# Performance work log

Measured on AMD Instinct MI355X. Metric: run time of the kernel, lower is better.

Reference implementation:

```python
import jax, jax.numpy as jnp
import numpy as np

D_MODEL = 1024
BULK_DIM = 10          # int(log2(d_model))
ADS_RADIUS = 1.0
B, N = 4, 2048


def setup_inputs() -> dict:
    key = jax.random.key(0)
    k1, k2 = jax.random.split(key, 2)
    boundary_tokens = jax.random.normal(k1, (B, N, D_MODEL), dtype=jnp.float32)
    W_b2b = jax.random.normal(k2, (D_MODEL, D_MODEL * BULK_DIM), dtype=jnp.float32) / np.sqrt(D_MODEL).astype(np.float32)
    b_b2b = jnp.zeros((D_MODEL * BULK_DIM,), dtype=jnp.float32)
    return {"boundary_tokens": boundary_tokens, "W_b2b": W_b2b, "b_b2b": b_b2b}


def _fast_marching(bulk_coords, ads_radius):
    # bulk_coords: (B, N, K, D). Sequential eikonal-style sweep through the
    # bulk depth z = 1..K; AdS warp factor L/z attenuates the front update
    # deeper into the bulk. Returns geodesics with the same shape.
    cz = jnp.moveaxis(bulk_coords, 2, 0)                 # (K, B, N, D)
    z = jnp.arange(1, bulk_coords.shape[2] + 1, dtype=bulk_coords.dtype)
    factors = ads_radius / z                             # (K,)

    def step(g, inp):
        c, f = inp
        g_new = g + f * (c - g)
        return g_new, g_new

    _, geos = jax.lax.scan(step, cz[0], (cz, factors))   # (K, B, N, D)
    return jnp.moveaxis(geos, 0, 2)                      # (B, N, K, D)


def reference(boundary_tokens, W_b2b, b_b2b):
    Bb, Nn, D = boundary_tokens.shape
    # boundary -> bulk linear projection, reshaped to (B, N, bulk_dim, D)
    bulk_coords = (boundary_tokens @ W_b2b + b_b2b).reshape(Bb, Nn, BULK_DIM, D)
    geodesics = _fast_marching(bulk_coords, ADS_RADIUS)  # (B, N, K, D)
    bulk_features = geodesics.mean(axis=2)               # (B, N, D)
    return bulk_features
```

## Files before the change

### kernel.cpp

```cpp
#include <hip/hip_runtime.h>
#include <stdint.h>


static constexpr float FW[10] = {
    0.2928968253968254f, 0.1928968253968254f, 0.1428968253968254f,
    0.1095634920634921f, 0.0845634920634921f, 0.0645634920634921f,
    0.0478968253968254f, 0.0336111111111111f, 0.0211111111111111f,
    0.0100000000000000f};

typedef __attribute__((ext_vector_type(8))) short short8;
typedef __attribute__((ext_vector_type(4))) float floatx4;

__device__ inline unsigned int bf16pack2(float hi, float lo) {
    unsigned int uh = __float_as_uint(hi) + 0x8000u;
    unsigned int ul = __float_as_uint(lo) + 0x8000u;
    return __builtin_amdgcn_perm(uh, ul, 0x07060302u);
}

#define LDS_AS(p) ((__attribute__((address_space(3))) unsigned int*)(p))
#define GLB_AS(p) ((const __attribute__((address_space(1))) unsigned int*)(p))

__global__ __launch_bounds__(256) void fold_w(const float* __restrict__ W,
                                              unsigned short* __restrict__ Wt) {
    __shared__ float T[64 * 65];
    const int t = threadIdx.x;
    const int n0 = blockIdx.x * 64;
    const int k0 = blockIdx.y * 64;

#pragma unroll
    for (int s = 0; s < 4; ++s) {
        int slot = s * 256 + t;
        int r = slot >> 4;
        int c4 = (slot & 15) * 4;
        const float4* src = (const float4*)(W + (size_t)(k0 + r) * 10240 + n0 + c4);
        float4 acc = {0.f, 0.f, 0.f, 0.f};
#pragma unroll
        for (int j = 0; j < 10; ++j) {
            float4 v = src[j * 256];
            acc.x += FW[j] * v.x; acc.y += FW[j] * v.y;
            acc.z += FW[j] * v.z; acc.w += FW[j] * v.w;
        }
        T[r * 65 + c4 + 0] = acc.x;
        T[r * 65 + c4 + 1] = acc.y;
        T[r * 65 + c4 + 2] = acc.z;
        T[r * 65 + c4 + 3] = acc.w;
    }
    __syncthreads();
#pragma unroll
    for (int s = 0; s < 4; ++s) {
        int slot = s * 256 + t;
        int nl = slot >> 4;
        int k4 = (slot & 15) * 4;
        float f0 = T[(k4 + 0) * 65 + nl];
        float f1 = T[(k4 + 1) * 65 + nl];
        float f2 = T[(k4 + 2) * 65 + nl];
        float f3 = T[(k4 + 3) * 65 + nl];
        uint2 p;
        p.x = bf16pack2(f1, f0);
        p.y = bf16pack2(f3, f2);
        *(uint2*)(Wt + (size_t)(n0 + nl) * 1024 + k0 + k4) = p;
    }
}

__global__ __launch_bounds__(256) void fold_b(const float* __restrict__ b,
                                              float* __restrict__ beff) {
    const int t = threadIdx.x;
    const float4* src = (const float4*)b + t;
    float4 acc = {0.f, 0.f, 0.f, 0.f};
#pragma unroll
    for (int j = 0; j < 10; ++j) {
        float4 v = src[j * 256];
        acc.x += FW[j] * v.x; acc.y += FW[j] * v.y;
        acc.z += FW[j] * v.z; acc.w += FW[j] * v.w;
    }
    ((float4*)beff)[t] = acc;
}

__global__ __launch_bounds__(256) void gemm_bf16(const float* __restrict__ A,
                                                 const unsigned short* __restrict__ Wt,
                                                 const float* __restrict__ beff,
                                                 float* __restrict__ C) {
    __shared__ __align__(16) unsigned short As[128 * 72];
    __shared__ __align__(16) unsigned char Bs[16384];

    const int t = threadIdx.x;
    const int lane = t & 63;
    const int w = t >> 6;
    const int quad = lane >> 4;
    const int l15 = lane & 15;
    const int wm = (w & 1) * 64;
    const int wn = (w >> 1) * 64;
    const int bm = blockIdx.y * 128;
    const int bn = blockIdx.x * 128;

    floatx4 acc[4][4];
#pragma unroll
    for (int i = 0; i < 4; ++i)
#pragma unroll
        for (int j = 0; j < 4; ++j) acc[i][j] = (floatx4){0.f, 0.f, 0.f, 0.f};

    const int ar = t >> 4;
    const int ac4 = (t & 15) * 4;
    const float* Abase = A + (size_t)(bm + ar) * 1024 + ac4;
    const char* WtB = (const char*)Wt;

    for (int k0 = 0; k0 < 1024; k0 += 64) {
#pragma unroll
        for (int i = 0; i < 4; ++i) {
            int I = w * 4 + i;
            int slot = I * 64 + lane;
            int nl = slot >> 3;
            int cs = slot & 7;
            int c = cs ^ (nl & 7);
            const char* g = WtB + (size_t)(bn + nl) * 2048 + k0 * 2 + c * 16;
            __builtin_amdgcn_global_load_lds(GLB_AS(g), LDS_AS(Bs + I * 1024), 16, 0, 0);
        }
        float4 av[8];
#pragma unroll
        for (int s = 0; s < 8; ++s)
            av[s] = *(const float4*)(Abase + (size_t)(s * 16) * 1024 + k0);
#pragma unroll
        for (int s = 0; s < 8; ++s) {
            uint2 p;
            p.x = bf16pack2(av[s].y, av[s].x);
            p.y = bf16pack2(av[s].w, av[s].z);
            *(uint2*)((char*)As + (size_t)(s * 16 + ar) * 144 + ac4 * 2) = p;
        }
        __syncthreads();

#pragma unroll
        for (int kk = 0; kk < 2; ++kk) {
            short8 af[4], bf[4];
#pragma unroll
            for (int tm = 0; tm < 4; ++tm) {
                int m = wm + tm * 16 + l15;
                af[tm] = *(const short8*)((const char*)As + (size_t)m * 144 + kk * 64 + quad * 16);
            }
#pragma unroll
            for (int tn = 0; tn < 4; ++tn) {
                int n = wn + tn * 16 + l15;
                int c = kk * 4 + quad;
                int slot = n * 8 + (c ^ (n & 7));
                bf[tn] = *(const short8*)(Bs + slot * 16);
            }
#pragma unroll
            for (int tm = 0; tm < 4; ++tm)
#pragma unroll
                for (int tn = 0; tn < 4; ++tn)
                    acc[tm][tn] = __builtin_amdgcn_mfma_f32_16x16x32_bf16(
                        af[tm], bf[tn], acc[tm][tn], 0, 0, 0);
        }
        __syncthreads();
    }

#pragma unroll
    for (int tn = 0; tn < 4; ++tn) {
        int col = bn + wn + tn * 16 + l15;
        float bias = beff[col];
#pragma unroll
        for (int tm = 0; tm < 4; ++tm) {
            int row0 = bm + wm + tm * 16 + quad * 4;
#pragma unroll
            for (int r = 0; r < 4; ++r)
                C[(size_t)(row0 + r) * 1024 + col] = acc[tm][tn][r] + bias;
        }
    }
}

extern "C" void kernel_launch(void* const* d_in, const int* in_sizes, int n_in,
                              void* d_out, int out_size, void* d_ws, size_t ws_size,
                              hipStream_t stream) {
    const float* tokens = (const float*)d_in[0];
    const float* W      = (const float*)d_in[1];
    const float* b      = (const float*)d_in[2];
    float* out = (float*)d_out;

    unsigned short* Wt = (unsigned short*)d_ws;
    float* beff = (float*)((char*)d_ws + 1024 * 1024 * 2);

    fold_w<<<dim3(16, 16), 256, 0, stream>>>(W, Wt);
    fold_b<<<1, 256, 0, stream>>>(b, beff);
    gemm_bf16<<<dim3(8, 64), 256, 0, stream>>>(tokens, Wt, beff, out);
}
```

Measured before the change: 143.3 us.

## Pre-convert activations to bf16 and load both GEMM operands via direct LDS loads

```diff
diff --git a/kernel.cpp b/kernel.cpp
--- a/kernel.cpp
+++ b/kernel.cpp
@@ -22,13 +22,13 @@
 
 __global__ __launch_bounds__(256) void fold_w(const float* __restrict__ W,
                                               unsigned short* __restrict__ Wt) {
-    __shared__ float T[64 * 65];
+    __shared__ float T[32 * 65];
     const int t = threadIdx.x;
     const int n0 = blockIdx.x * 64;
-    const int k0 = blockIdx.y * 64;
-
-#pragma unroll
-    for (int s = 0; s < 4; ++s) {
+    const int k0 = blockIdx.y * 32;
+
+#pragma unroll
+    for (int s = 0; s < 2; ++s) {
         int slot = s * 256 + t;
         int r = slot >> 4;
         int c4 = (slot & 15) * 4;
@@ -47,10 +47,10 @@
     }
     __syncthreads();
 #pragma unroll
-    for (int s = 0; s < 4; ++s) {
+    for (int s = 0; s < 2; ++s) {
         int slot = s * 256 + t;
-        int nl = slot >> 4;
-        int k4 = (slot & 15) * 4;
+        int nl = slot >> 3;
+        int k4 = (slot & 7) * 4;
         float f0 = T[(k4 + 0) * 65 + nl];
         float f1 = T[(k4 + 1) * 65 + nl];
         float f2 = T[(k4 + 2) * 65 + nl];
@@ -76,10 +76,102 @@
     ((float4*)beff)[t] = acc;
 }
 
-__global__ __launch_bounds__(256) void gemm_bf16(const float* __restrict__ A,
+__global__ __launch_bounds__(256) void cvt_bf16(const float* __restrict__ A,
+                                                uint4* __restrict__ Ab) {
+    size_t i = (size_t)blockIdx.x * 256 + threadIdx.x;
+    const float4* src = (const float4*)A + i * 2;
+    float4 a0 = src[0], a1 = src[1];
+    uint4 p;
+    p.x = bf16pack2(a0.y, a0.x);
+    p.y = bf16pack2(a0.w, a0.z);
+    p.z = bf16pack2(a1.y, a1.x);
+    p.w = bf16pack2(a1.w, a1.z);
+    Ab[i] = p;
+}
+
+__global__ __launch_bounds__(256) void gemm_bf16(const unsigned short* __restrict__ Ab,
                                                  const unsigned short* __restrict__ Wt,
                                                  const float* __restrict__ beff,
                                                  float* __restrict__ C) {
+    __shared__ __align__(16) unsigned char As[16384];
+    __shared__ __align__(16) unsigned char Bs[16384];
+
+    const int t = threadIdx.x;
+    const int lane = t & 63;
+    const int w = t >> 6;
+    const int quad = lane >> 4;
+    const int l15 = lane & 15;
+    const int wm = (w & 1) * 64;
+    const int wn = (w >> 1) * 64;
+    const int bm = blockIdx.x * 128;
+    const int bn = blockIdx.y * 128;
+
+    floatx4 acc[4][4];
+#pragma unroll
+    for (int i = 0; i < 4; ++i)
+#pragma unroll
+        for (int j = 0; j < 4; ++j) acc[i][j] = (floatx4){0.f, 0.f, 0.f, 0.f};
+
+    const char* Abase = (const char*)Ab + (size_t)bm * 2048;
+    const char* Bbase = (const char*)Wt + (size_t)bn * 2048;
+
+    for (int k0 = 0; k0 < 1024; k0 += 64) {
+#pragma unroll
+        for (int i = 0; i < 4; ++i) {
+            int I = w * 4 + i;
+            int slot = I * 64 + lane;
+            int m = slot >> 3;
+            int c = (slot & 7) ^ (m & 7);
+            size_t off = (size_t)m * 2048 + (size_t)k0 * 2 + c * 16;
+            __builtin_amdgcn_global_load_lds(GLB_AS(Abase + off), LDS_AS(As + I * 1024), 16, 0, 0);
+            __builtin_amdgcn_global_load_lds(GLB_AS(Bbase + off), LDS_AS(Bs + I * 1024), 16, 0, 0);
+        }
+        __syncthreads();
+
+#pragma unroll
+        for (int kk = 0; kk < 2; ++kk) {
+            short8 af[4], bf[4];
+            int c = kk * 4 + quad;
+#pragma unroll
+            for (int tm = 0; tm < 4; ++tm) {
+                int m = wm + tm * 16 + l15;
+                int slot = m * 8 + (c ^ (m & 7));
+                af[tm] = *(const short8*)(As + slot * 16);
+            }
+#pragma unroll
+            for (int tn = 0; tn < 4; ++tn) {
+                int n = wn + tn * 16 + l15;
+                int slot = n * 8 + (c ^ (n & 7));
+                bf[tn] = *(const short8*)(Bs + slot * 16);
+            }
+#pragma unroll
+            for (int tm = 0; tm < 4; ++tm)
+#pragma unroll
+                for (int tn = 0; tn < 4; ++tn)
+                    acc[tm][tn] = __builtin_amdgcn_mfma_f32_16x16x32_bf16(
+                        af[tm], bf[tn], acc[tm][tn], 0, 0, 0);
+        }
+        __syncthreads();
+    }
+
+#pragma unroll
+    for (int tn = 0; tn < 4; ++tn) {
+        int col = bn + wn + tn * 16 + l15;
+        float bias = beff[col];
+#pragma unroll
+        for (int tm = 0; tm < 4; ++tm) {
+            int row0 = bm + wm + tm * 16 + quad * 4;
+#pragma unroll
+            for (int r = 0; r < 4; ++r)
+                C[(size_t)(row0 + r) * 1024 + col] = acc[tm][tn][r] + bias;
+        }
+    }
+}
+
+__global__ __launch_bounds__(256) void gemm_fb(const float* __restrict__ A,
+                                               const unsigned short* __restrict__ Wt,
+                                               const float* __restrict__ beff,
+                                               float* __restrict__ C) {
     __shared__ __align__(16) unsigned short As[128 * 72];
     __shared__ __align__(16) unsigned char Bs[16384];
 
@@ -110,8 +202,7 @@
             int I = w * 4 + i;
             int slot = I * 64 + lane;
             int nl = slot >> 3;
-            int cs = slot & 7;
-            int c = cs ^ (nl & 7);
+            int c = (slot & 7) ^ (nl & 7);
             const char* g = WtB + (size_t)(bn + nl) * 2048 + k0 * 2 + c * 16;
             __builtin_amdgcn_global_load_lds(GLB_AS(g), LDS_AS(Bs + I * 1024), 16, 0, 0);
         }
@@ -127,7 +218,6 @@
             *(uint2*)((char*)As + (size_t)(s * 16 + ar) * 144 + ac4 * 2) = p;
         }
         __syncthreads();
-
 #pragma unroll
         for (int kk = 0; kk < 2; ++kk) {
             short8 af[4], bf[4];
@@ -152,7 +242,6 @@
         }
         __syncthreads();
     }
-
 #pragma unroll
     for (int tn = 0; tn < 4; ++tn) {
         int col = bn + wn + tn * 16 + l15;
@@ -176,9 +265,16 @@
     float* out = (float*)d_out;
 
     unsigned short* Wt = (unsigned short*)d_ws;
-    float* beff = (float*)((char*)d_ws + 1024 * 1024 * 2);
-
-    fold_w<<<dim3(16, 16), 256, 0, stream>>>(W, Wt);
+    float* beff = (float*)((char*)d_ws + 2097152);
+    unsigned short* Ab = (unsigned short*)((char*)d_ws + 2101248);
+
+    fold_w<<<dim3(16, 32), 256, 0, stream>>>(W, Wt);
     fold_b<<<1, 256, 0, stream>>>(b, beff);
-    gemm_bf16<<<dim3(8, 64), 256, 0, stream>>>(tokens, Wt, beff, out);
-}
+
+    if (ws_size >= 2101248 + (size_t)8192 * 1024 * 2) {
+        cvt_bf16<<<4096, 256, 0, stream>>>(tokens, (uint4*)Ab);
+        gemm_bf16<<<dim3(64, 8), 256, 0, stream>>>(Ab, Wt, beff, out);
+    } else {
+        gemm_fb<<<dim3(8, 64), 256, 0, stream>>>(tokens, Wt, beff, out);
+    }
+}
```

Measured after the change: 135.8 us. 5.2% less time.
